# Kernel tuning notes

Hardware: AMD Instinct MI355X
Metric: run time of the kernel (lower is better)

The kernel has to match this reference:

```python
import jax, jax.numpy as jnp
import numpy as np

N = 100000   # nodes
E = 1600000  # edges (avg degree 16)
F = 256      # in_channels
H = 4        # heads
C = 32       # out_channels per head
NEG_SLOPE = 0.2  # PyG GATConv default leaky_relu slope


def setup_inputs() -> dict:
    key = jax.random.key(0)
    k0, k1, k2, k3, k4 = jax.random.split(key, 5)
    x = jax.random.normal(k0, (N, F), dtype=jnp.float32)
    edge_index = jax.random.randint(k1, (2, E), 0, N, dtype=jnp.int32)
    W = jax.random.normal(k2, (F, H * C), dtype=jnp.float32) * 0.05
    att_src = jax.random.normal(k3, (H, C), dtype=jnp.float32) * 0.05
    att_dst = jax.random.normal(k4, (H, C), dtype=jnp.float32) * 0.05
    bias = jnp.zeros((H * C,), dtype=jnp.float32)
    return {"x": x, "edge_index": edge_index, "W": W,
            "att_src": att_src, "att_dst": att_dst, "bias": bias}


def reference(x, edge_index, W, att_src, att_dst, bias):
    n = x.shape[0]
    h_, c_ = att_src.shape
    # add self loops (PyG default add_self_loops=True)
    loops = jnp.arange(n, dtype=edge_index.dtype)
    src = jnp.concatenate([edge_index[0], loops])  # source node j of each edge
    dst = jnp.concatenate([edge_index[1], loops])  # target node i of each edge
    # linear projection, per-head view: [N, H, C]
    h = (x @ W).reshape(n, h_, c_)
    # per-node attention halves: [N, H]
    a_src = jnp.einsum('nhc,hc->nh', h, att_src)
    a_dst = jnp.einsum('nhc,hc->nh', h, att_dst)
    # per-edge logits with leaky relu: [Etot, H]
    e = jax.nn.leaky_relu(a_src[src] + a_dst[dst], NEG_SLOPE)
    # segment softmax over edges sharing the same destination
    m = jax.ops.segment_max(e, dst, num_segments=n)
    m = jnp.where(jnp.isfinite(m), m, jnp.zeros_like(m))  # isolated nodes
    p = jnp.exp(e - m[dst])
    s = jax.ops.segment_sum(p, dst, num_segments=n)
    alpha = p / (s[dst] + 1e-16)  # [Etot, H]
    # weighted scatter-aggregate of source features
    msg = h[src] * alpha[:, :, None]  # [Etot, H, C]
    out = jax.ops.segment_sum(msg, dst, num_segments=n)  # [N, H, C]
    return out.reshape(n, h_ * c_) + bias
```

## Files before the change

### kernel.cpp

```cpp
#include <hip/hip_runtime.h>

#define NEG_SLOPE 0.2f
#define CAP 64
#define NPART 8

typedef __attribute__((ext_vector_type(8))) short short8;
typedef __attribute__((ext_vector_type(4))) float f32x4;

__device__ __forceinline__ float lrelu(float x) {
    return x > 0.0f ? x : NEG_SLOPE * x;
}

__device__ __forceinline__ unsigned short f2bf(float f) {
    unsigned int u = __float_as_uint(f);
    u += 0x7FFFu + ((u >> 16) & 1u);
    return (unsigned short)(u >> 16);
}

__device__ __forceinline__ float2 bfpair(unsigned int u) {
    float2 r;
    r.x = __uint_as_float(u << 16);
    r.y = __uint_as_float(u & 0xFFFF0000u);
    return r;
}

__global__ void convW_kernel(const float* __restrict__ W, unsigned short* __restrict__ Wtf) {
    int idx = blockIdx.x * blockDim.x + threadIdx.x;
    int j = idx & 7;
    int lane = (idx >> 3) & 63;
    int f = idx >> 9;
    int t = f >> 3;
    int ks = f & 7;
    int k = ks * 32 + (lane >> 4) * 8 + j;
    int nn = t * 16 + (lane & 15);
    Wtf[idx] = f2bf(W[k * 128 + nn]);
}

#define XS_STRIDE 280
__global__ __launch_bounds__(256) void gemm_fused_kernel(
    const float* __restrict__ x, const unsigned short* __restrict__ Wtf,
    const float* __restrict__ att_src, const float* __restrict__ att_dst,
    unsigned short* __restrict__ hb, float* __restrict__ a_src,
    float* __restrict__ a_dst, int n) {
    __shared__ unsigned short xs[64 * XS_STRIDE];
    int tid = threadIdx.x;
    int row0 = blockIdx.x * 64;

    #pragma unroll
    for (int it = 0; it < 16; ++it) {
        int flat = tid * 4 + it * 1024;
        int r = flat >> 8;
        int c = flat & 255;
        int gr = row0 + r;
        if (gr >= n) gr = n - 1;
        float4 v = *(const float4*)&x[(size_t)gr * 256 + c];
        unsigned short b0 = f2bf(v.x), b1 = f2bf(v.y), b2 = f2bf(v.z), b3 = f2bf(v.w);
        unsigned short* dp = &xs[r * XS_STRIDE + c];
        dp[0] = b0; dp[1] = b1; dp[2] = b2; dp[3] = b3;
    }
    __syncthreads();

    int wave = tid >> 6;
    int lane = tid & 63;
    int ln = lane & 15;
    int quad = lane >> 4;
    int row0w = row0 + wave * 16;

    f32x4 acc[8];
    #pragma unroll
    for (int t = 0; t < 8; ++t) acc[t] = (f32x4){0.f, 0.f, 0.f, 0.f};

    #pragma unroll
    for (int ks = 0; ks < 8; ++ks) {
        short8 afrag = *(const short8*)&xs[(wave * 16 + ln) * XS_STRIDE + ks * 32 + quad * 8];
        #pragma unroll
        for (int t = 0; t < 8; ++t) {
            short8 bfrag = *(const short8*)&Wtf[(((t * 8 + ks) * 64) + lane) * 8];
            acc[t] = __builtin_amdgcn_mfma_f32_16x16x32_bf16(afrag, bfrag, acc[t], 0, 0, 0);
        }
    }

    #pragma unroll
    for (int t = 0; t < 8; ++t) {
        #pragma unroll
        for (int r = 0; r < 4; ++r) {
            int grow = row0w + quad * 4 + r;
            if (grow < n) hb[(size_t)grow * 128 + t * 16 + ln] = f2bf(acc[t][r]);
        }
    }

    #pragma unroll
    for (int hd = 0; hd < 4; ++hd) {
        float as1 = att_src[hd * 32 + ln];
        float as2 = att_src[hd * 32 + 16 + ln];
        float ad1 = att_dst[hd * 32 + ln];
        float ad2 = att_dst[hd * 32 + 16 + ln];
        #pragma unroll
        for (int r = 0; r < 4; ++r) {
            float ps = acc[2 * hd][r] * as1 + acc[2 * hd + 1][r] * as2;
            float pd = acc[2 * hd][r] * ad1 + acc[2 * hd + 1][r] * ad2;
            #pragma unroll
            for (int off = 1; off < 16; off <<= 1) {
                ps += __shfl_xor(ps, off);
                pd += __shfl_xor(pd, off);
            }
            if (ln == 0) {
                int grow = row0w + quad * 4 + r;
                if (grow < n) {
                    a_src[grow * 4 + hd] = ps;
                    a_dst[grow * 4 + hd] = pd;
                }
            }
        }
    }
}

__global__ __launch_bounds__(256) void build_kernel(
    const int* __restrict__ src, const int* __restrict__ dst,
    int* __restrict__ deg, int* __restrict__ bucket, int e, int n) {
    int p = blockIdx.x & (NPART - 1);
    int slice = blockIdx.x >> 3;
    int nslices = gridDim.x >> 3;
    int part = (n + NPART - 1) / NPART;
    unsigned lo = (unsigned)(p * part);
    int e4 = e >> 2;
    int stride = nslices * 256;
    const int4* dst4 = (const int4*)dst;
    const int4* src4 = (const int4*)src;
    for (int i = slice * 256 + threadIdx.x; i < e4; i += stride) {
        int4 d4 = dst4[i];
        int4 s4 = src4[i];
        if ((unsigned)(d4.x - lo) < (unsigned)part) {
            int r = atomicAdd(&deg[d4.x], 1);
            if (r < CAP) bucket[d4.x * CAP + r] = s4.x;
        }
        if ((unsigned)(d4.y - lo) < (unsigned)part) {
            int r = atomicAdd(&deg[d4.y], 1);
            if (r < CAP) bucket[d4.y * CAP + r] = s4.y;
        }
        if ((unsigned)(d4.z - lo) < (unsigned)part) {
            int r = atomicAdd(&deg[d4.z], 1);
            if (r < CAP) bucket[d4.z * CAP + r] = s4.z;
        }
        if ((unsigned)(d4.w - lo) < (unsigned)part) {
            int r = atomicAdd(&deg[d4.w], 1);
            if (r < CAP) bucket[d4.w * CAP + r] = s4.w;
        }
    }
    if (blockIdx.x == 0 && threadIdx.x < (e & 3)) {
        int i = e4 * 4 + threadIdx.x;
        int d = dst[i];
        int r = atomicAdd(&deg[d], 1);
        if (r < CAP) bucket[d * CAP + r] = src[i];
    }
}

__global__ __launch_bounds__(256) void aggregate_kernel(
    const unsigned short* __restrict__ hb, const float* __restrict__ a_src,
    const float* __restrict__ a_dst, const int* __restrict__ deg,
    const int* __restrict__ bucket, const float* __restrict__ bias,
    float* __restrict__ out, int n) {
    __shared__ float lds_alpha[4][CAP][4];
    __shared__ int lds_s[4][CAP];
    int wave = threadIdx.x >> 6;
    int lane = threadIdx.x & 63;
    int node = blockIdx.x * 4 + wave;
    if (node >= n) node = n - 1;
    int el = lane & 15;
    int hh = lane >> 4;

    int cnt = deg[node];
    if (cnt > CAP) cnt = CAP;

    float adst = a_dst[node * 4 + hh];
    float e_self = lrelu(a_src[node * 4 + hh] + adst);

    float e_gp[4];
    int s_gp[4];
    float mloc = e_self;
    #pragma unroll
    for (int g = 0; g < 4; ++g) {
        int p = g * 16 + el;
        if (p < cnt) {
            int s = bucket[node * CAP + p];
            s_gp[g] = s;
            float ev = lrelu(a_src[s * 4 + hh] + adst);
            e_gp[g] = ev;
            mloc = fmaxf(mloc, ev);
        } else {
            s_gp[g] = node;
            e_gp[g] = -INFINITY;
        }
    }
    #pragma unroll
    for (int off = 1; off < 16; off <<= 1)
        mloc = fmaxf(mloc, __shfl_xor(mloc, off));

    float pe_gp[4];
    float dloc = 0.0f;
    #pragma unroll
    for (int g = 0; g < 4; ++g) {
        float pe = __expf(e_gp[g] - mloc);
        pe_gp[g] = pe;
        dloc += pe;
    }
    #pragma unroll
    for (int off = 1; off < 16; off <<= 1)
        dloc += __shfl_xor(dloc, off);

    float pe_self = __expf(e_self - mloc);
    float inv = 1.0f / (dloc + pe_self);
    float alpha_self = pe_self * inv;

    #pragma unroll
    for (int g = 0; g < 4; ++g) {
        lds_alpha[wave][g * 16 + el][hh] = pe_gp[g] * inv;
        if (hh == 0) lds_s[wave][g * 16 + el] = s_gp[g];
    }
    __syncthreads();

    const unsigned int* hbu = (const unsigned int*)hb;
    float2 acc;
    {
        float2 hv = bfpair(hbu[(unsigned)node * 64u + lane]);
        acc.x = alpha_self * hv.x;
        acc.y = alpha_self * hv.y;
    }
    int p = 0;
    for (; p + 4 <= cnt; p += 4) {
        int s0 = lds_s[wave][p + 0];
        int s1 = lds_s[wave][p + 1];
        int s2 = lds_s[wave][p + 2];
        int s3 = lds_s[wave][p + 3];
        float al0 = lds_alpha[wave][p + 0][hh];
        float al1 = lds_alpha[wave][p + 1][hh];
        float al2 = lds_alpha[wave][p + 2][hh];
        float al3 = lds_alpha[wave][p + 3][hh];
        unsigned int v0 = hbu[(unsigned)s0 * 64u + lane];
        unsigned int v1 = hbu[(unsigned)s1 * 64u + lane];
        unsigned int v2 = hbu[(unsigned)s2 * 64u + lane];
        unsigned int v3 = hbu[(unsigned)s3 * 64u + lane];
        float2 h0 = bfpair(v0), h1 = bfpair(v1), h2 = bfpair(v2), h3 = bfpair(v3);
        acc.x += al0 * h0.x + al1 * h1.x + al2 * h2.x + al3 * h3.x;
        acc.y += al0 * h0.y + al1 * h1.y + al2 * h2.y + al3 * h3.y;
    }
    for (; p < cnt; ++p) {
        int s = lds_s[wave][p];
        float al = lds_alpha[wave][p][hh];
        float2 hv = bfpair(hbu[(unsigned)s * 64u + lane]);
        acc.x += al * hv.x;
        acc.y += al * hv.y;
    }

    int oc = hh * 32 + el * 2;
    float2 b2 = *(const float2*)&bias[oc];
    float2 o;
    o.x = acc.x + b2.x;
    o.y = acc.y + b2.y;
    *(float2*)&out[(size_t)node * 128 + oc] = o;
}

extern "C" void kernel_launch(void* const* d_in, const int* in_sizes, int n_in,
                              void* d_out, int out_size, void* d_ws, size_t ws_size,
                              hipStream_t stream) {
    const float* x = (const float*)d_in[0];
    const int* edge_index = (const int*)d_in[1];
    const float* W = (const float*)d_in[2];
    const float* att_src = (const float*)d_in[3];
    const float* att_dst = (const float*)d_in[4];
    const float* bias = (const float*)d_in[5];
    float* out = (float*)d_out;

    int n = in_sizes[0] / 256;
    int e = in_sizes[1] / 2;
    const int* esrc = edge_index;
    const int* edst = edge_index + e;

    char* w = (char*)d_ws;
    unsigned short* hb = (unsigned short*)w;  w += (size_t)n * 128 * 2;
    float* a_src = (float*)w;                 w += (size_t)n * 4 * 4;
    float* a_dst = (float*)w;                 w += (size_t)n * 4 * 4;
    unsigned short* Wtf = (unsigned short*)w; w += 128 * 256 * 2;
    int* deg = (int*)w;                       w += (size_t)n * 4;
    int* bucket = (int*)w;                    w += (size_t)n * CAP * 4;

    hipMemsetAsync(deg, 0, (size_t)n * sizeof(int), stream);

    convW_kernel<<<128, 256, 0, stream>>>(W, Wtf);
    gemm_fused_kernel<<<(n + 63) / 64, 256, 0, stream>>>(x, Wtf, att_src, att_dst,
                                                         hb, a_src, a_dst, n);
    build_kernel<<<256 * NPART, 256, 0, stream>>>(esrc, edst, deg, bucket, e, n);
    aggregate_kernel<<<(n + 3) / 4, 256, 0, stream>>>(hb, a_src, a_dst, deg,
                                                      bucket, bias, out, n);
}
```

Measured before the change: 377.6 us.

## Stage W in LDS, load x rows directly, and unroll gather by eight

The GEMM kernel now puts the whole bf16 weight fragment array in shared memory and reads x rows straight from global memory into MFMA A fragments. Each wave computes 32 rows (two 16-row tiles), so every B fragment is reused across two MFMAs and the grid is halved. The aggregation loop is unrolled to eight neighbours, with vectorized int4 index loads from LDS, to keep more gathers in flight. The trade-off is 64 KB of LDS per block, which limits occupancy, plus more accumulator registers.

```diff
diff --git a/kernel.cpp b/kernel.cpp
--- a/kernel.cpp
+++ b/kernel.cpp
@@ -36,27 +36,18 @@
     Wtf[idx] = f2bf(W[k * 128 + nn]);
 }
 
-#define XS_STRIDE 280
 __global__ __launch_bounds__(256) void gemm_fused_kernel(
     const float* __restrict__ x, const unsigned short* __restrict__ Wtf,
     const float* __restrict__ att_src, const float* __restrict__ att_dst,
     unsigned short* __restrict__ hb, float* __restrict__ a_src,
     float* __restrict__ a_dst, int n) {
-    __shared__ unsigned short xs[64 * XS_STRIDE];
+    __shared__ unsigned short Bs[32768];
     int tid = threadIdx.x;
-    int row0 = blockIdx.x * 64;
 
     #pragma unroll
     for (int it = 0; it < 16; ++it) {
-        int flat = tid * 4 + it * 1024;
-        int r = flat >> 8;
-        int c = flat & 255;
-        int gr = row0 + r;
-        if (gr >= n) gr = n - 1;
-        float4 v = *(const float4*)&x[(size_t)gr * 256 + c];
-        unsigned short b0 = f2bf(v.x), b1 = f2bf(v.y), b2 = f2bf(v.z), b3 = f2bf(v.w);
-        unsigned short* dp = &xs[r * XS_STRIDE + c];
-        dp[0] = b0; dp[1] = b1; dp[2] = b2; dp[3] = b3;
+        int o = (it * 256 + tid) * 8;
+        *(short8*)&Bs[o] = *(const short8*)&Wtf[o];
     }
     __syncthreads();
 
@@ -64,28 +55,52 @@
     int lane = tid & 63;
     int ln = lane & 15;
     int quad = lane >> 4;
-    int row0w = row0 + wave * 16;
-
-    f32x4 acc[8];
-    #pragma unroll
-    for (int t = 0; t < 8; ++t) acc[t] = (f32x4){0.f, 0.f, 0.f, 0.f};
+    int row0w = blockIdx.x * 128 + wave * 32;
+
+    int r0 = row0w + ln;       if (r0 >= n) r0 = n - 1;
+    int r1 = row0w + 16 + ln;  if (r1 >= n) r1 = n - 1;
+    const float* xr0 = &x[(size_t)r0 * 256];
+    const float* xr1 = &x[(size_t)r1 * 256];
+
+    f32x4 acc[2][8];
+    #pragma unroll
+    for (int rt = 0; rt < 2; ++rt)
+        #pragma unroll
+        for (int t = 0; t < 8; ++t) acc[rt][t] = (f32x4){0.f, 0.f, 0.f, 0.f};
 
     #pragma unroll
     for (int ks = 0; ks < 8; ++ks) {
-        short8 afrag = *(const short8*)&xs[(wave * 16 + ln) * XS_STRIDE + ks * 32 + quad * 8];
+        int ko = ks * 32 + quad * 8;
+        float4 a00 = *(const float4*)&xr0[ko];
+        float4 a01 = *(const float4*)&xr0[ko + 4];
+        float4 a10 = *(const float4*)&xr1[ko];
+        float4 a11 = *(const float4*)&xr1[ko + 4];
+        short8 af0, af1;
+        af0[0] = (short)f2bf(a00.x); af0[1] = (short)f2bf(a00.y);
+        af0[2] = (short)f2bf(a00.z); af0[3] = (short)f2bf(a00.w);
+        af0[4] = (short)f2bf(a01.x); af0[5] = (short)f2bf(a01.y);
+        af0[6] = (short)f2bf(a01.z); af0[7] = (short)f2bf(a01.w);
+        af1[0] = (short)f2bf(a10.x); af1[1] = (short)f2bf(a10.y);
+        af1[2] = (short)f2bf(a10.z); af1[3] = (short)f2bf(a10.w);
+        af1[4] = (short)f2bf(a11.x); af1[5] = (short)f2bf(a11.y);
+        af1[6] = (short)f2bf(a11.z); af1[7] = (short)f2bf(a11.w);
         #pragma unroll
         for (int t = 0; t < 8; ++t) {
-            short8 bfrag = *(const short8*)&Wtf[(((t * 8 + ks) * 64) + lane) * 8];
-            acc[t] = __builtin_amdgcn_mfma_f32_16x16x32_bf16(afrag, bfrag, acc[t], 0, 0, 0);
-        }
-    }
-
-    #pragma unroll
-    for (int t = 0; t < 8; ++t) {
+            short8 bf = *(const short8*)&Bs[(((t * 8 + ks) * 64) + lane) * 8];
+            acc[0][t] = __builtin_amdgcn_mfma_f32_16x16x32_bf16(af0, bf, acc[0][t], 0, 0, 0);
+            acc[1][t] = __builtin_amdgcn_mfma_f32_16x16x32_bf16(af1, bf, acc[1][t], 0, 0, 0);
+        }
+    }
+
+    #pragma unroll
+    for (int rt = 0; rt < 2; ++rt) {
         #pragma unroll
-        for (int r = 0; r < 4; ++r) {
-            int grow = row0w + quad * 4 + r;
-            if (grow < n) hb[(size_t)grow * 128 + t * 16 + ln] = f2bf(acc[t][r]);
+        for (int t = 0; t < 8; ++t) {
+            #pragma unroll
+            for (int r = 0; r < 4; ++r) {
+                int grow = row0w + rt * 16 + quad * 4 + r;
+                if (grow < n) hb[(size_t)grow * 128 + t * 16 + ln] = f2bf(acc[rt][t][r]);
+            }
         }
     }
 
@@ -96,19 +111,22 @@
         float ad1 = att_dst[hd * 32 + ln];
         float ad2 = att_dst[hd * 32 + 16 + ln];
         #pragma unroll
-        for (int r = 0; r < 4; ++r) {
-            float ps = acc[2 * hd][r] * as1 + acc[2 * hd + 1][r] * as2;
-            float pd = acc[2 * hd][r] * ad1 + acc[2 * hd + 1][r] * ad2;
+        for (int rt = 0; rt < 2; ++rt) {
             #pragma unroll
-            for (int off = 1; off < 16; off <<= 1) {
-                ps += __shfl_xor(ps, off);
-                pd += __shfl_xor(pd, off);
-            }
-            if (ln == 0) {
-                int grow = row0w + quad * 4 + r;
-                if (grow < n) {
-                    a_src[grow * 4 + hd] = ps;
-                    a_dst[grow * 4 + hd] = pd;
+            for (int r = 0; r < 4; ++r) {
+                float ps = acc[rt][2 * hd][r] * as1 + acc[rt][2 * hd + 1][r] * as2;
+                float pd = acc[rt][2 * hd][r] * ad1 + acc[rt][2 * hd + 1][r] * ad2;
+                #pragma unroll
+                for (int off = 1; off < 16; off <<= 1) {
+                    ps += __shfl_xor(ps, off);
+                    pd += __shfl_xor(pd, off);
+                }
+                if (ln == 0) {
+                    int grow = row0w + rt * 16 + quad * 4 + r;
+                    if (grow < n) {
+                        a_src[grow * 4 + hd] = ps;
+                        a_dst[grow * 4 + hd] = pd;
+                    }
                 }
             }
         }
@@ -182,7 +200,7 @@
     for (int g = 0; g < 4; ++g) {
         int p = g * 16 + el;
         if (p < cnt) {
-            int s = bucket[node * CAP + p];
+            int s = bucket[(unsigned)node * CAP + p];
             s_gp[g] = s;
             float ev = lrelu(a_src[s * 4 + hh] + adst);
             e_gp[g] = ev;
@@ -227,19 +245,42 @@
         acc.y = alpha_self * hv.y;
     }
     int p = 0;
-    for (; p + 4 <= cnt; p += 4) {
-        int s0 = lds_s[wave][p + 0];
-        int s1 = lds_s[wave][p + 1];
-        int s2 = lds_s[wave][p + 2];
-        int s3 = lds_s[wave][p + 3];
+    for (; p + 8 <= cnt; p += 8) {
+        int4 sA = *(const int4*)&lds_s[wave][p];
+        int4 sB = *(const int4*)&lds_s[wave][p + 4];
+        unsigned int v0 = hbu[(unsigned)sA.x * 64u + lane];
+        unsigned int v1 = hbu[(unsigned)sA.y * 64u + lane];
+        unsigned int v2 = hbu[(unsigned)sA.z * 64u + lane];
+        unsigned int v3 = hbu[(unsigned)sA.w * 64u + lane];
+        unsigned int v4 = hbu[(unsigned)sB.x * 64u + lane];
+        unsigned int v5 = hbu[(unsigned)sB.y * 64u + lane];
+        unsigned int v6 = hbu[(unsigned)sB.z * 64u + lane];
+        unsigned int v7 = hbu[(unsigned)sB.w * 64u + lane];
         float al0 = lds_alpha[wave][p + 0][hh];
         float al1 = lds_alpha[wave][p + 1][hh];
         float al2 = lds_alpha[wave][p + 2][hh];
         float al3 = lds_alpha[wave][p + 3][hh];
-        unsigned int v0 = hbu[(unsigned)s0 * 64u + lane];
-        unsigned int v1 = hbu[(unsigned)s1 * 64u + lane];
-        unsigned int v2 = hbu[(unsigned)s2 * 64u + lane];
-        unsigned int v3 = hbu[(unsigned)s3 * 64u + lane];
+        float al4 = lds_alpha[wave][p + 4][hh];
+        float al5 = lds_alpha[wave][p + 5][hh];
+        float al6 = lds_alpha[wave][p + 6][hh];
+        float al7 = lds_alpha[wave][p + 7][hh];
+        float2 h0 = bfpair(v0), h1 = bfpair(v1), h2 = bfpair(v2), h3 = bfpair(v3);
+        float2 h4 = bfpair(v4), h5 = bfpair(v5), h6 = bfpair(v6), h7 = bfpair(v7);
+        acc.x += al0 * h0.x + al1 * h1.x + al2 * h2.x + al3 * h3.x
+               + al4 * h4.x + al5 * h5.x + al6 * h6.x + al7 * h7.x;
+        acc.y += al0 * h0.y + al1 * h1.y + al2 * h2.y + al3 * h3.y
+               + al4 * h4.y + al5 * h5.y + al6 * h6.y + al7 * h7.y;
+    }
+    for (; p + 4 <= cnt; p += 4) {
+        int4 sA = *(const int4*)&lds_s[wave][p];
+        unsigned int v0 = hbu[(unsigned)sA.x * 64u + lane];
+        unsigned int v1 = hbu[(unsigned)sA.y * 64u + lane];
+        unsigned int v2 = hbu[(unsigned)sA.z * 64u + lane];
+        unsigned int v3 = hbu[(unsigned)sA.w * 64u + lane];
+        float al0 = lds_alpha[wave][p + 0][hh];
+        float al1 = lds_alpha[wave][p + 1][hh];
+        float al2 = lds_alpha[wave][p + 2][hh];
+        float al3 = lds_alpha[wave][p + 3][hh];
         float2 h0 = bfpair(v0), h1 = bfpair(v1), h2 = bfpair(v2), h3 = bfpair(v3);
         acc.x += al0 * h0.x + al1 * h1.x + al2 * h2.x + al3 * h3.x;
         acc.y += al0 * h0.y + al1 * h1.y + al2 * h2.y + al3 * h3.y;
@@ -287,8 +328,8 @@
     hipMemsetAsync(deg, 0, (size_t)n * sizeof(int), stream);
 
     convW_kernel<<<128, 256, 0, stream>>>(W, Wtf);
-    gemm_fused_kernel<<<(n + 63) / 64, 256, 0, stream>>>(x, Wtf, att_src, att_dst,
-                                                         hb, a_src, a_dst, n);
+    gemm_fused_kernel<<<(n + 127) / 128, 256, 0, stream>>>(x, Wtf, att_src, att_dst,
+                                                           hb, a_src, a_dst, n);
     build_kernel<<<256 * NPART, 256, 0, stream>>>(esrc, edst, deg, bucket, e, n);
     aggregate_kernel<<<(n + 3) / 4, 256, 0, stream>>>(hb, a_src, a_dst, deg,
                                                       bucket, bias, out, n);
```

After: 357.1 us. -5.4%, faster.
